# Kernel optimization log

Hardware: AMD Instinct MI355X
Metric: run time of the kernel (lower is better)

The kernel has to match this reference:

```python
import jax, jax.numpy as jnp
import numpy as np

GRID = (128, 128, 128)  # (D, H, W) from init_kwargs
B = 16
P = 16384  # num_points
THRESHOLD = 0.0  # forward default


def setup_inputs() -> dict:
    key = jax.random.key(0)
    k1, k2, k3, k4 = jax.random.split(key, 4)
    D, H, W = GRID
    voxels = jax.random.uniform(k1, (B, 1, D, H, W), dtype=jnp.float32)  # occupancies in (0,1)
    mins = jax.random.normal(k2, (B, 3), dtype=jnp.float32)
    ranges = jax.random.uniform(k3, (B, 3), dtype=jnp.float32) + 0.5  # positive ranges
    jitter = jax.random.uniform(k4, (B, P, 3), dtype=jnp.float32)  # torch.rand_like(coords)
    return {"voxels": voxels, "mins": mins, "ranges": ranges, "jitter": jitter, "num_points": P}


def reference(voxels, mins, ranges, jitter, num_points):
    # voxels: (B, 1, D, H, W); mins/ranges: (B, 3); jitter: (B, num_points, 3)
    Bn = voxels.shape[0]
    D, H, W = voxels.shape[2], voxels.shape[3], voxels.shape[4]
    flat = voxels.reshape(Bn, D * H * W)
    # active = weights > threshold; inputs guarantee active_count >= num_points,
    # so the original module always takes the deterministic top-k branch.
    masked = jnp.where(flat > THRESHOLD, flat, -jnp.inf)
    _, chosen = jax.lax.top_k(masked, num_points)  # (B, P) flat voxel indices
    dz = H * W
    dy = W
    iz = chosen // dz
    iy = (chosen % dz) // dy
    ix = chosen % dy
    coords = jnp.stack([iz, iy, ix], axis=-1).astype(voxels.dtype)  # (B, P, 3)
    grid = jnp.array([D, H, W], dtype=voxels.dtype)
    coords = (coords + jitter) / grid
    points = coords * ranges[:, None, :] + mins[:, None, :]  # (B, P, 3)
    return points
```

## Files before the change

kernel.cpp:

```cpp
#include <hip/hip_runtime.h>
#include <stdint.h>

#define BATCH 16
#define NVOX (128*128*128)
#define KSEL 16384
#define XB1 64
#define PBCAP 1024
#define T0BITS 0x3F7B0000u
#define FSH2 7
#define NBIN 2560
#define NSPLIT 16
#define RWIN 1024
#define SCAP 1280
#define EQCAP 512

typedef unsigned long long u64;


__global__ __launch_bounds__(256) void k_pass1(const float* __restrict__ vox,
                                               uint32_t* __restrict__ privh,
                                               u64* __restrict__ prelist,
                                               uint32_t* __restrict__ pcnts) {
  const int b = blockIdx.y, xb = blockIdx.x;
  const int tid = threadIdx.x;
  __shared__ uint32_t lh[NBIN];
  __shared__ u64 pbuf[PBCAP];
  __shared__ uint32_t pcnt;
  for (int i = tid; i < NBIN; i += 256) lh[i] = 0;
  if (tid == 0) pcnt = 0;
  __syncthreads();
  const float4* v4 = (const float4*)(vox + (size_t)b * NVOX);
  const int q = NVOX / 16;

#define PROC(f, idx) do {                                                      \
    const int bi = __float_as_int(f);                                          \
    if (bi >= (int)T0BITS) {                                                   \
      const uint32_t bits = (uint32_t)bi;                                      \
      atomicAdd(&lh[(bits - T0BITS) >> FSH2], 1u);                             \
      const uint32_t p = atomicAdd(&pcnt, 1u);                                 \
      if (p < (uint32_t)PBCAP)                                                 \
        pbuf[p] = ((u64)bits << 32) | (u64)(0xFFFFFFFFu - (uint32_t)(idx));    \
    } } while (0)

  for (int i = xb * 256 + tid; i < q; i += XB1 * 256) {
    const float4 v0 = v4[i];
    const float4 v1 = v4[i + q];
    const float4 v2 = v4[i + 2 * q];
    const float4 v3 = v4[i + 3 * q];
    PROC(v0.x, 4*i+0);         PROC(v0.y, 4*i+1);
    PROC(v0.z, 4*i+2);         PROC(v0.w, 4*i+3);
    PROC(v1.x, 4*(i+q)+0);     PROC(v1.y, 4*(i+q)+1);
    PROC(v1.z, 4*(i+q)+2);     PROC(v1.w, 4*(i+q)+3);
    PROC(v2.x, 4*(i+2*q)+0);   PROC(v2.y, 4*(i+2*q)+1);
    PROC(v2.z, 4*(i+2*q)+2);   PROC(v2.w, 4*(i+2*q)+3);
    PROC(v3.x, 4*(i+3*q)+0);   PROC(v3.y, 4*(i+3*q)+1);
    PROC(v3.z, 4*(i+3*q)+2);   PROC(v3.w, 4*(i+3*q)+3);
  }
#undef PROC
  __syncthreads();
  const uint32_t np = min(pcnt, (uint32_t)PBCAP);
  u64* slice = prelist + ((size_t)(b * XB1 + xb) << 10);
  for (uint32_t i = tid; i < np; i += 256) slice[i] = pbuf[i];
  if (tid == 0) pcnts[b * XB1 + xb] = np;
  uint32_t* hp = privh + (size_t)(b * XB1 + xb) * NBIN;
  for (int i = tid; i < NBIN; i += 256) hp[i] = lh[i];
}

__global__ __launch_bounds__(256) void k_reduce(const uint32_t* __restrict__ privh,
                                                uint32_t* __restrict__ fh) {
  const int b = blockIdx.y, g = blockIdx.x;
  const int tid = threadIdx.x;
  const int bin = g * 64 + (tid & 63);
  __shared__ uint32_t red[256];
  uint32_t s = 0;
  for (int xb = (tid >> 6); xb < XB1; xb += 4)
    s += privh[(size_t)(b * XB1 + xb) * NBIN + bin];
  red[tid] = s;
  __syncthreads();
  if (tid < 64)
    fh[(size_t)b * NBIN + g * 64 + tid] =
        red[tid] + red[tid + 64] + red[tid + 128] + red[tid + 192];
}

__global__ __launch_bounds__(1024) void k_cut(const uint32_t* __restrict__ fh,
                                              uint32_t* __restrict__ ctrl,
                                              uint32_t* __restrict__ gcur,
                                              uint32_t* __restrict__ rbase,
                                              uint32_t* __restrict__ eqcnt) {
  const int b = blockIdx.x;
  const int tid = threadIdx.x;
  __shared__ uint32_t cnt[NBIN];
  __shared__ uint32_t cur[NBIN];
  __shared__ uint32_t sbuf[1024];
  __shared__ uint32_t sL, sCgt;
  for (int i = tid; i < NBIN; i += 1024) cnt[i] = fh[(size_t)b * NBIN + i];
  __syncthreads();
  const int B0 = tid * 3;
  const uint32_t c0 = (B0 < NBIN) ? cnt[B0] : 0u;
  const uint32_t c1 = (B0 + 1 < NBIN) ? cnt[B0 + 1] : 0u;
  const uint32_t c2 = (B0 + 2 < NBIN) ? cnt[B0 + 2] : 0u;
  const uint32_t my = c0 + c1 + c2;
  sbuf[tid] = my;
  __syncthreads();
  for (int off = 1; off < 1024; off <<= 1) {
    uint32_t v = (tid + off < 1024) ? sbuf[tid + off] : 0u;
    __syncthreads();
    sbuf[tid] += v;
    __syncthreads();
  }
  const uint32_t sufExcl = sbuf[tid] - my;
  const uint32_t cu2 = sufExcl;
  const uint32_t cu1 = sufExcl + c2;
  const uint32_t cu0 = cu1 + c1;
  if (B0 < NBIN) cur[B0] = cu0;
  if (B0 + 1 < NBIN) cur[B0 + 1] = cu1;
  if (B0 + 2 < NBIN) cur[B0 + 2] = cu2;
  if (B0 < NBIN && cu0 < (uint32_t)KSEL && cu0 + c0 >= (uint32_t)KSEL) { sL = (uint32_t)B0; sCgt = cu0; }
  if (B0 + 1 < NBIN && cu1 < (uint32_t)KSEL && cu1 + c1 >= (uint32_t)KSEL) { sL = (uint32_t)(B0 + 1); sCgt = cu1; }
  if (B0 + 2 < NBIN && cu2 < (uint32_t)KSEL && cu2 + c2 >= (uint32_t)KSEL) { sL = (uint32_t)(B0 + 2); sCgt = cu2; }
  __syncthreads();
  const uint32_t Cgt = sCgt;
  for (int i = tid; i < NBIN; i += 1024) gcur[(size_t)b * NBIN + i] = cur[i];
#pragma unroll
  for (int k = 0; k < 3; ++k) {
    const int B = B0 + k;
    if (B < NBIN) {
      const uint32_t cb = cur[B];
      const uint32_t cp = (B == 0) ? 0xFFFFFFFFu : cur[B - 1];
      for (uint32_t m = cb / RWIN + 1u; m <= 15u && (u64)m * RWIN <= (u64)cp; ++m)
        rbase[b * 17 + m] = min(cp, Cgt);
    }
  }
  if (tid == 0) {
    rbase[b * 17 + 0] = 0;
    rbase[b * 17 + 16] = Cgt;
    ctrl[b * 4 + 0] = Cgt;
    ctrl[b * 4 + 1] = sL;
    eqcnt[b] = 0;
  }
}

__global__ __launch_bounds__(256) void k_scatter(const u64* __restrict__ prelist,
                                                 const uint32_t* __restrict__ pcnts,
                                                 const uint32_t* __restrict__ ctrl,
                                                 uint32_t* __restrict__ gcur,
                                                 u64* __restrict__ ranked,
                                                 u64* __restrict__ eqg,
                                                 uint32_t* __restrict__ eqcnt) {
  const int b = blockIdx.y, xb = blockIdx.x;
  const int tid = threadIdx.x;
  const uint32_t L = ctrl[b * 4 + 1];
  const uint32_t TloB = T0BITS + (L << FSH2);
  const uint32_t ThiB = TloB + (1u << FSH2);
  const uint32_t n = pcnts[b * XB1 + xb];
  const u64* slice = prelist + ((size_t)(b * XB1 + xb) << 10);
  for (uint32_t i = tid; i < n; i += 256) {
    const u64 key = slice[i];
    const uint32_t bits = (uint32_t)(key >> 32);
    if (bits >= ThiB) {
      const uint32_t B = (bits - T0BITS) >> FSH2;
      const uint32_t pos = atomicAdd(&gcur[(size_t)b * NBIN + B], 1u);
      if (pos < (uint32_t)KSEL) ranked[(size_t)b * KSEL + pos] = key;
    } else if (bits >= TloB) {
      const uint32_t e = atomicAdd(&eqcnt[b], 1u);
      if (e < (uint32_t)EQCAP) eqg[(size_t)b * EQCAP + e] = key;
    }
  }
}

#define EMIT(key_, rank_) do {                                                \
    const uint32_t idx_ = 0xFFFFFFFFu - (uint32_t)(key_);                     \
    const float iz_ = (float)(idx_ >> 14);                                    \
    const float iy_ = (float)((idx_ >> 7) & 127u);                            \
    const float ix_ = (float)(idx_ & 127u);                                   \
    const float* jt_ = jitter + ((size_t)b * KSEL + (rank_)) * 3;             \
    float* o_ = out + ((size_t)b * KSEL + (rank_)) * 3;                       \
    o_[0] = (iz_ + jt_[0]) * inv * rg0 + mn0;                                 \
    o_[1] = (iy_ + jt_[1]) * inv * rg1 + mn1;                                 \
    o_[2] = (ix_ + jt_[2]) * inv * rg2 + mn2;                                 \
  } while (0)

__global__ __launch_bounds__(256) void k_bsort(const u64* __restrict__ ranked,
                                               const uint32_t* __restrict__ rbase,
                                               const uint32_t* __restrict__ ctrl,
                                               const uint32_t* __restrict__ gcur,
                                               const u64* __restrict__ eqg,
                                               const uint32_t* __restrict__ eqcnt,
                                               const float* __restrict__ mins,
                                               const float* __restrict__ ranges,
                                               const float* __restrict__ jitter,
                                               float* __restrict__ out) {
  const int b = blockIdx.y, s = blockIdx.x;
  const int tid = threadIdx.x;
  __shared__ u64 sk[SCAP];
  __shared__ u64 sk2[SCAP];
  __shared__ u64 eqs[EQCAP];
  const uint32_t Cgt = ctrl[b * 4 + 0];
  const uint32_t rb0 = min(rbase[b * 17 + s], Cgt);
  const uint32_t rb1 = min(rbase[b * 17 + s + 1], Cgt);
  const uint32_t tot = (rb1 > rb0) ? min(rb1 - rb0, (uint32_t)SCAP) : 0u;
  const u64* rk = ranked + (size_t)b * KSEL + rb0;
  const uint32_t* gc = gcur + (size_t)b * NBIN;
  for (uint32_t r = (uint32_t)tid; r < tot; r += 256) sk[r] = rk[r];
  __syncthreads();
  for (uint32_t r = (uint32_t)tid; r < tot; r += 256) {
    const u64 key = sk[r];
    const uint32_t B = ((uint32_t)(key >> 32) - T0BITS) >> FSH2;
    const uint32_t lo = (B + 1u < (uint32_t)NBIN) ? gc[B + 1] : 0u;
    const uint32_t hi = gc[B];
    const uint32_t jlo = lo - rb0;
    const uint32_t jhi = min(hi - rb0, tot);
    uint32_t rnk = 0;
    for (uint32_t j = jlo; j < jhi; ++j) rnk += (sk[j] > key) ? 1u : 0u;
    sk2[jlo + rnk] = key;
  }
  __syncthreads();
  const float mn0 = mins[b * 3 + 0], mn1 = mins[b * 3 + 1], mn2 = mins[b * 3 + 2];
  const float rg0 = ranges[b * 3 + 0], rg1 = ranges[b * 3 + 1], rg2 = ranges[b * 3 + 2];
  const float inv = 1.0f / 128.0f;
  for (uint32_t r = (uint32_t)tid; r < tot; r += 256) EMIT(sk2[r], rb0 + r);
  const uint32_t loR = (uint32_t)s * (uint32_t)RWIN;
  const uint32_t hiR = loR + (uint32_t)RWIN;
  if (hiR > Cgt) {
    const uint32_t n = min(eqcnt[b], (uint32_t)EQCAP);
    uint32_t p2 = 1; while (p2 < n) p2 <<= 1;
    for (uint32_t i = (uint32_t)tid; i < p2; i += 256)
      eqs[i] = (i < n) ? eqg[(size_t)b * EQCAP + i] : 0ull;
    __syncthreads();
    for (uint32_t kk = 2; kk <= p2; kk <<= 1) {
      for (uint32_t j = kk >> 1; j > 0; j >>= 1) {
        for (uint32_t i = (uint32_t)tid; i < p2; i += 256) {
          const uint32_t l = i ^ j;
          if (l > i) {
            const u64 a = eqs[i], c = eqs[l];
            if (((i & kk) == 0) ? (a < c) : (a > c)) { eqs[i] = c; eqs[l] = a; }
          }
        }
        __syncthreads();
      }
    }
    const uint32_t r0 = max(Cgt, loR);
    for (uint32_t rank = r0 + (uint32_t)tid; rank < hiR; rank += 256) {
      const uint32_t e = rank - Cgt;
      if (e < n) EMIT(eqs[e], rank);
    }
  }
}

extern "C" void kernel_launch(void* const* d_in, const int* in_sizes, int n_in,
                              void* d_out, int out_size, void* d_ws, size_t ws_size,
                              hipStream_t stream) {
  const float* vox    = (const float*)d_in[0];
  const float* mins   = (const float*)d_in[1];
  const float* ranges = (const float*)d_in[2];
  const float* jitter = (const float*)d_in[3];
  float* out = (float*)d_out;

  char* ws = (char*)d_ws;
  uint32_t* privh   = (uint32_t*)(ws + 0);
  uint32_t* pcnts   = (uint32_t*)(ws + 10485760);
  uint32_t* fh      = (uint32_t*)(ws + 10489856);
  uint32_t* gcur    = (uint32_t*)(ws + 10653696);
  uint32_t* rbase   = (uint32_t*)(ws + 10817536);
  uint32_t* ctrl    = (uint32_t*)(ws + 10821632);
  uint32_t* eqcnt   = (uint32_t*)(ws + 10822656);
  u64*      eqg     = (u64*)(ws + 10823680);
  u64*      ranked  = (u64*)(ws + 10889216);
  u64*      prelist = (u64*)(ws + 12986368);
  if (ws_size < 21374976) return;

  k_pass1  <<<dim3(XB1, BATCH), 256, 0, stream>>>(vox, privh, prelist, pcnts);
  k_reduce <<<dim3(NBIN / 64, BATCH), 256, 0, stream>>>(privh, fh);
  k_cut    <<<BATCH, 1024, 0, stream>>>(fh, ctrl, gcur, rbase, eqcnt);
  k_scatter<<<dim3(XB1, BATCH), 256, 0, stream>>>(prelist, pcnts, ctrl, gcur,
                                                  ranked, eqg, eqcnt);
  k_bsort  <<<dim3(NSPLIT, BATCH), 256, 0, stream>>>(ranked, rbase, ctrl, gcur, eqg, eqcnt,
                                                     mins, ranges, jitter, out);
}
```

Measured before the change: 69.72 us.

## Replace private histograms with global atomics and use wave-shuffle suffix scan

The pass-1 kernel now increments a zero-initialised global histogram directly with atomics instead of building per-block shared histograms that a separate reduce kernel summed. This removes the k_reduce launch and the write and read of the per-block private histograms, and shrinks the workspace. The k_cut suffix scan now uses wavefront shuffles plus a small per-wave sum array instead of a ten-step shared-memory scan with barriers. The cost is global atomic contention on hot bins across 64 blocks per batch, plus an added memset.

```diff
diff --git a/kernel.cpp b/kernel.cpp
--- a/kernel.cpp
+++ b/kernel.cpp
@@ -18,25 +18,24 @@
 
 
 __global__ __launch_bounds__(256) void k_pass1(const float* __restrict__ vox,
-                                               uint32_t* __restrict__ privh,
+                                               uint32_t* __restrict__ fh,
                                                u64* __restrict__ prelist,
                                                uint32_t* __restrict__ pcnts) {
   const int b = blockIdx.y, xb = blockIdx.x;
   const int tid = threadIdx.x;
-  __shared__ uint32_t lh[NBIN];
   __shared__ u64 pbuf[PBCAP];
   __shared__ uint32_t pcnt;
-  for (int i = tid; i < NBIN; i += 256) lh[i] = 0;
   if (tid == 0) pcnt = 0;
   __syncthreads();
   const float4* v4 = (const float4*)(vox + (size_t)b * NVOX);
+  uint32_t* fhb = fh + (size_t)b * NBIN;
   const int q = NVOX / 16;
 
 #define PROC(f, idx) do {                                                      \
     const int bi = __float_as_int(f);                                          \
     if (bi >= (int)T0BITS) {                                                   \
       const uint32_t bits = (uint32_t)bi;                                      \
-      atomicAdd(&lh[(bits - T0BITS) >> FSH2], 1u);                             \
+      atomicAdd(&fhb[(bits - T0BITS) >> FSH2], 1u);       \
       const uint32_t p = atomicAdd(&pcnt, 1u);                                 \
       if (p < (uint32_t)PBCAP)                                                 \
         pbuf[p] = ((u64)bits << 32) | (u64)(0xFFFFFFFFu - (uint32_t)(idx));    \
@@ -62,24 +61,6 @@
   u64* slice = prelist + ((size_t)(b * XB1 + xb) << 10);
   for (uint32_t i = tid; i < np; i += 256) slice[i] = pbuf[i];
   if (tid == 0) pcnts[b * XB1 + xb] = np;
-  uint32_t* hp = privh + (size_t)(b * XB1 + xb) * NBIN;
-  for (int i = tid; i < NBIN; i += 256) hp[i] = lh[i];
-}
-
-__global__ __launch_bounds__(256) void k_reduce(const uint32_t* __restrict__ privh,
-                                                uint32_t* __restrict__ fh) {
-  const int b = blockIdx.y, g = blockIdx.x;
-  const int tid = threadIdx.x;
-  const int bin = g * 64 + (tid & 63);
-  __shared__ uint32_t red[256];
-  uint32_t s = 0;
-  for (int xb = (tid >> 6); xb < XB1; xb += 4)
-    s += privh[(size_t)(b * XB1 + xb) * NBIN + bin];
-  red[tid] = s;
-  __syncthreads();
-  if (tid < 64)
-    fh[(size_t)b * NBIN + g * 64 + tid] =
-        red[tid] + red[tid + 64] + red[tid + 128] + red[tid + 192];
 }
 
 __global__ __launch_bounds__(1024) void k_cut(const uint32_t* __restrict__ fh,
@@ -89,9 +70,10 @@
                                               uint32_t* __restrict__ eqcnt) {
   const int b = blockIdx.x;
   const int tid = threadIdx.x;
+  const int lane = tid & 63, wv = tid >> 6;
   __shared__ uint32_t cnt[NBIN];
   __shared__ uint32_t cur[NBIN];
-  __shared__ uint32_t sbuf[1024];
+  __shared__ uint32_t wsum[16];
   __shared__ uint32_t sL, sCgt;
   for (int i = tid; i < NBIN; i += 1024) cnt[i] = fh[(size_t)b * NBIN + i];
   __syncthreads();
@@ -100,15 +82,17 @@
   const uint32_t c1 = (B0 + 1 < NBIN) ? cnt[B0 + 1] : 0u;
   const uint32_t c2 = (B0 + 2 < NBIN) ? cnt[B0 + 2] : 0u;
   const uint32_t my = c0 + c1 + c2;
-  sbuf[tid] = my;
-  __syncthreads();
-  for (int off = 1; off < 1024; off <<= 1) {
-    uint32_t v = (tid + off < 1024) ? sbuf[tid + off] : 0u;
-    __syncthreads();
-    sbuf[tid] += v;
-    __syncthreads();
-  }
-  const uint32_t sufExcl = sbuf[tid] - my;
+  uint32_t ss = my;
+#pragma unroll
+  for (int off = 1; off < 64; off <<= 1) {
+    const uint32_t up = __shfl_down(ss, off, 64);
+    if (lane + off < 64) ss += up;
+  }
+  if (lane == 0) wsum[wv] = ss;
+  __syncthreads();
+  uint32_t wsuf = 0;
+  for (int w = wv + 1; w < 16; ++w) wsuf += wsum[w];
+  const uint32_t sufExcl = (ss - my) + wsuf;
   const uint32_t cu2 = sufExcl;
   const uint32_t cu1 = sufExcl + c2;
   const uint32_t cu0 = cu1 + c1;
@@ -257,20 +241,20 @@
   float* out = (float*)d_out;
 
   char* ws = (char*)d_ws;
-  uint32_t* privh   = (uint32_t*)(ws + 0);
-  uint32_t* pcnts   = (uint32_t*)(ws + 10485760);
-  uint32_t* fh      = (uint32_t*)(ws + 10489856);
-  uint32_t* gcur    = (uint32_t*)(ws + 10653696);
-  uint32_t* rbase   = (uint32_t*)(ws + 10817536);
-  uint32_t* ctrl    = (uint32_t*)(ws + 10821632);
-  uint32_t* eqcnt   = (uint32_t*)(ws + 10822656);
-  u64*      eqg     = (u64*)(ws + 10823680);
-  u64*      ranked  = (u64*)(ws + 10889216);
-  u64*      prelist = (u64*)(ws + 12986368);
-  if (ws_size < 21374976) return;
-
-  k_pass1  <<<dim3(XB1, BATCH), 256, 0, stream>>>(vox, privh, prelist, pcnts);
-  k_reduce <<<dim3(NBIN / 64, BATCH), 256, 0, stream>>>(privh, fh);
+  uint32_t* fh      = (uint32_t*)(ws + 0);
+  uint32_t* gcur    = (uint32_t*)(ws + 163840);
+  uint32_t* pcnts   = (uint32_t*)(ws + 327680);
+  uint32_t* ctrl    = (uint32_t*)(ws + 331776);
+  uint32_t* rbase   = (uint32_t*)(ws + 332800);
+  uint32_t* eqcnt   = (uint32_t*)(ws + 336896);
+  u64*      eqg     = (u64*)(ws + 337920);
+  u64*      ranked  = (u64*)(ws + 403456);
+  u64*      prelist = (u64*)(ws + 2500608);
+  if (ws_size < 10889216) return;
+
+  hipMemsetAsync(fh, 0, 163840, stream);
+
+  k_pass1  <<<dim3(XB1, BATCH), 256, 0, stream>>>(vox, fh, prelist, pcnts);
   k_cut    <<<BATCH, 1024, 0, stream>>>(fh, ctrl, gcur, rbase, eqcnt);
   k_scatter<<<dim3(XB1, BATCH), 256, 0, stream>>>(prelist, pcnts, ctrl, gcur,
                                                   ranked, eqg, eqcnt);
```

Result: slower. 78.38 us (+12.4%).
